# Kernel tuning notes

Measured on AMD Instinct MI355X. Metric: run time of the kernel, lower is better.

## Reference

```python
import jax, jax.numpy as jnp
import numpy as np

NX = 320   # image matrix (nRead)
NC = 8     # coils
NT = 8     # motion states
M = 65536  # non-Cartesian k-space samples per frame
OS = 2     # gridding oversampling factor


def setup_inputs() -> dict:
    key = jax.random.key(0)
    ks = jax.random.split(key, 7)
    kspace_r = jax.random.normal(ks[0], (NC, M), jnp.float32)
    kspace_i = jax.random.normal(ks[1], (NC, M), jnp.float32)
    # k-space trajectory normalized to [-0.5, 0.5)
    traj = jax.random.uniform(ks[2], (M, 2, NT), jnp.float32, -0.5, 0.5)
    csm_r = jax.random.normal(ks[3], (NC, NX, NX), jnp.float32)
    csm_i = jax.random.normal(ks[4], (NC, NX, NX), jnp.float32)
    dcf = jax.random.uniform(ks[5], (M, NT), jnp.float32)
    # motion/flow field in pixels, [NX, NX, 2, NT]
    motions = 3.0 * jax.random.normal(ks[6], (NX, NX, 2, NT), jnp.float32)
    return dict(kspace_r=kspace_r, kspace_i=kspace_i, traj=traj,
                csm_r=csm_r, csm_i=csm_i, dcf=dcf, motions=motions)


def _grid_adjoint(kspace, traj_t, dcf_t, csm):
    """Adjoint NUFFT (gpuNUFFT adj_op): density-compensated bilinear gridding
    onto a 2x oversampled Cartesian grid, inverse FFT, center crop,
    deapodization, and conjugate coil combination."""
    G = OS * NX
    data = (kspace * dcf_t[None, :]).astype(jnp.complex64)  # [NC, M]
    u = (traj_t[:, 0] + 0.5) * G
    v = (traj_t[:, 1] + 0.5) * G
    u0 = jnp.floor(u)
    v0 = jnp.floor(v)
    du = (u - u0).astype(jnp.float32)
    dv = (v - v0).astype(jnp.float32)
    i0 = u0.astype(jnp.int32) % G
    i1 = (i0 + 1) % G
    j0 = v0.astype(jnp.int32) % G
    j1 = (j0 + 1) % G
    grid = jnp.zeros((NC, G, G), jnp.complex64)
    grid = grid.at[:, i0, j0].add(data * ((1.0 - du) * (1.0 - dv)))
    grid = grid.at[:, i1, j0].add(data * (du * (1.0 - dv)))
    grid = grid.at[:, i0, j1].add(data * ((1.0 - du) * dv))
    grid = grid.at[:, i1, j1].add(data * (du * dv))
    im_os = jnp.fft.fftshift(
        jnp.fft.ifft2(jnp.fft.ifftshift(grid, axes=(-2, -1)), axes=(-2, -1)),
        axes=(-2, -1))
    s = (G - NX) // 2
    im = im_os[:, s:s + NX, s:s + NX]  # [NC, NX, NX]
    # deapodization: FT of the triangle (bilinear) gridding kernel is sinc^2
    x = (jnp.arange(NX, dtype=jnp.float32) - NX // 2) / G
    d = jnp.sinc(x) ** 2
    im = im / (d[:, None] * d[None, :])
    # conjugate coil combine with sensitivity maps
    return jnp.sum(jnp.conj(csm) * im, axis=0).astype(jnp.complex64)


def _bilinear_warp(im, flow):
    """apply_sparse_motion: sparse bilinear-interpolation warp of a 2D image
    by a per-pixel displacement field flow[..., 0:2] (in pixels)."""
    Nx, Ny = im.shape
    xs = jnp.arange(Nx, dtype=jnp.float32)[:, None] + flow[..., 0]
    ys = jnp.arange(Ny, dtype=jnp.float32)[None, :] + flow[..., 1]
    xs = jnp.clip(xs, 0.0, Nx - 1.0)
    ys = jnp.clip(ys, 0.0, Ny - 1.0)
    x0 = jnp.floor(xs).astype(jnp.int32)
    y0 = jnp.floor(ys).astype(jnp.int32)
    x1 = jnp.minimum(x0 + 1, Nx - 1)
    y1 = jnp.minimum(y0 + 1, Ny - 1)
    dx = xs - x0.astype(jnp.float32)
    dy = ys - y0.astype(jnp.float32)
    return ((1.0 - dx) * (1.0 - dy) * im[x0, y0]
            + dx * (1.0 - dy) * im[x1, y0]
            + (1.0 - dx) * dy * im[x0, y1]
            + dx * dy * im[x1, y1])


def reference(kspace_r, kspace_i, traj, csm_r, csm_i, dcf, motions):
    kspace = (kspace_r + 1j * kspace_i).astype(jnp.complex64)
    csm = (csm_r + 1j * csm_i).astype(jnp.complex64)

    def frame(traj_t, dcf_t, flow_t):
        im = _grid_adjoint(kspace, traj_t, dcf_t, csm)
        return _bilinear_warp(im, flow_t)

    # vmap over motion states: traj[..., t], dcf[..., t], motions[..., t]
    per_frame = jax.vmap(frame, in_axes=(2, 1, 3))(traj, dcf, motions)  # [NT, NX, NX]
    out = jnp.sum(per_frame, axis=0)  # temporal sum, complex [NX, NX]
    return jnp.stack([out.real, out.imag], axis=-1)  # [NX, NX, 2]
```

## Files before the change

### kernel.cpp

```cpp
#include <hip/hip_runtime.h>
#include <math.h>

#define NXI 320
#define NCI 8
#define NTI 8
#define MI  65536
#define GI  640
#define G2I (GI*GI)
#define NPIX (NXI*NXI)
#define REC_F 20
#define NBINS (NTI*G2I)
#define SCAN_BLKS (NBINS/1024)

typedef float v2f __attribute__((ext_vector_type(2)));

__device__ inline v2f cmul(v2f a, v2f b) {
    v2f axx = __builtin_shufflevector(a, a, 0, 0);
    v2f ayy = __builtin_shufflevector(a, a, 1, 1);
    v2f byx = __builtin_shufflevector(b, b, 1, 0);
    v2f r = axx * b;
    v2f t = ayy * byx;
    return r + v2f{-t.x, t.y};
}

__device__ inline v2f shfl_xor_v(v2f v, int m) {
    return v2f{__shfl_xor(v.x, m, 64), __shfl_xor(v.y, m, 64)};
}

__device__ inline void cell_of(const float* __restrict__ traj, int m, int f,
                               int& i0s, int& j0s, float& du, float& dv)
{
    float tu = traj[(m*2 + 0)*NTI + f];
    float tv = traj[(m*2 + 1)*NTI + f];
    float u = (tu + 0.5f) * (float)GI;
    float v = (tv + 0.5f) * (float)GI;
    float fu = floorf(u), fv = floorf(v);
    du = u - fu; dv = v - fv;
    i0s = (int)fu + GI/2; if (i0s >= GI) i0s -= GI;
    j0s = (int)fv + GI/2; if (j0s >= GI) j0s -= GI;
}

__global__ __launch_bounds__(256) void count_cells(
    const float* __restrict__ traj, int* __restrict__ counts)
{
    int tid = blockIdx.x * 256 + threadIdx.x;
    int f = tid >> 16, m = tid & (MI - 1);
    int i0s, j0s; float du, dv;
    cell_of(traj, m, f, i0s, j0s, du, dv);
    atomicAdd(&counts[f*G2I + i0s*GI + j0s], 1);
}

__device__ inline int scan1024(int v, int tid, int* tmp) {
    tmp[tid] = v; __syncthreads();
    for (int d = 1; d < 1024; d <<= 1) {
        int y = (tid >= d) ? tmp[tid - d] : 0;
        __syncthreads();
        tmp[tid] += y;
        __syncthreads();
    }
    return tmp[tid];
}

__global__ __launch_bounds__(1024) void scanA(const int* __restrict__ counts,
                                              int* __restrict__ binstart,
                                              int* __restrict__ sums)
{
    __shared__ int tmp[1024];
    int tid = threadIdx.x;
    int i = blockIdx.x * 1024 + tid;
    int v = counts[i];
    int incl = scan1024(v, tid, tmp);
    binstart[i] = incl - v;
    if (tid == 1023) sums[blockIdx.x] = incl;
}

__global__ __launch_bounds__(1024) void scanB(int* __restrict__ sums)
{
    __shared__ int tmp[1024];
    int tid = threadIdx.x;
    int base = tid * 4;
    int v[4]; int s = 0;
    #pragma unroll
    for (int q = 0; q < 4; ++q) {
        int idx = base + q;
        v[q] = (idx < SCAN_BLKS) ? sums[idx] : 0;
        s += v[q];
    }
    int incl = scan1024(s, tid, tmp);
    int run = incl - s;
    #pragma unroll
    for (int q = 0; q < 4; ++q) {
        int idx = base + q;
        if (idx < SCAN_BLKS) sums[idx] = run;
        run += v[q];
    }
}

__global__ __launch_bounds__(1024) void scanC(int* __restrict__ binstart,
                                              const int* __restrict__ sums,
                                              int* __restrict__ cursor)
{
    int i = blockIdx.x * 1024 + threadIdx.x;
    int v = binstart[i] + sums[blockIdx.x];
    binstart[i] = v;
    cursor[i] = v;
    if (i == NBINS - 1) binstart[NBINS] = NTI * MI;
}

__global__ __launch_bounds__(256) void scatter_cells(
    const float* __restrict__ kr, const float* __restrict__ ki,
    const float* __restrict__ traj, const float* __restrict__ dcf,
    int* __restrict__ cursor, float* __restrict__ recs)
{
    int tid = blockIdx.x * 256 + threadIdx.x;
    int f = tid >> 16, m = tid & (MI - 1);
    int i0s, j0s; float du, dv;
    cell_of(traj, m, f, i0s, j0s, du, dv);
    float w = dcf[m*NTI + f];
    int slot = atomicAdd(&cursor[f*G2I + i0s*GI + j0s], 1);
    float4* r = (float4*)(recs + (size_t)slot * REC_F);
    r[0] = make_float4(du, dv, 0.f, 0.f);
    #pragma unroll
    for (int q = 0; q < 4; ++q) {
        int c0 = 2*q;
        r[1+q] = make_float4(kr[c0*MI + m]*w,     ki[c0*MI + m]*w,
                             kr[(c0+1)*MI + m]*w, ki[(c0+1)*MI + m]*w);
    }
}

__device__ inline void dft5p(v2f x0, v2f x1, v2f x2, v2f x3, v2f x4, v2f* X)
{
    const float c1 = 0.309016994f, c2 = -0.809016994f;
    const float s1 = 0.951056516f, s2 =  0.587785252f;
    v2f S1 = x1 + x4, D1 = x1 - x4;
    v2f S2 = x2 + x3, D2 = x2 - x3;
    X[0] = x0 + S1 + S2;
    v2f A = x0 + c1*S1 + c2*S2;
    v2f T = s1*D1 + s2*D2;
    v2f B = x0 + c2*S1 + c1*S2;
    v2f U = s2*D1 - s1*D2;
    v2f iT = v2f{-T.y, T.x};
    v2f iU = v2f{-U.y, U.x};
    X[1] = A + iT;  X[4] = A - iT;
    X[2] = B + iU;  X[3] = B - iU;
}

__device__ inline void fft640_pruned(v2f* a, int lane, v2f* line, int xorm)
{
    const float PI = 3.14159265358979f;
    #pragma unroll
    for (int s = 0; s < 6; ++s) {
        const int h = 32 >> s;
        bool low = (lane & h) == 0;
        int k = (lane << s) & 63;
        float sn, cs;
        __sincosf((2.0f * PI / 64.0f) * (float)k, &sn, &cs);
        v2f ws = v2f{cs, sn};
        #pragma unroll
        for (int n = 0; n < 10; ++n) {
            v2f p = shfl_xor_v(a[n], h);
            v2f tl = p + a[n];
            v2f th = cmul(a[n] - p, ws);
            a[n] = low ? tl : th;
        }
    }
    int k1 = __brev(lane) >> 26;
    float th2 = (2.0f * PI / 640.0f) * (float)k1;
    float sn, cs;
    __sincosf(th2, &sn, &cs);
    v2f wb = v2f{cs, sn};
    v2f w = wb;
    #pragma unroll
    for (int n = 1; n < 10; ++n) {
        a[n] = cmul(a[n], w);
        w = cmul(w, wb);
    }
    v2f E[5], O[5];
    dft5p(a[0], a[2], a[4], a[6], a[8], E);
    dft5p(a[1], a[3], a[5], a[7], a[9], O);
    const v2f tk1 = { 0.809016994f, 0.587785252f};
    const v2f tk2 = { 0.309016994f, 0.951056516f};
    const v2f tk3 = {-0.309016994f, 0.951056516f};
    const v2f tk4 = {-0.809016994f, 0.587785252f};
    v2f t1 = cmul(tk1, O[1]);
    v2f t2 = cmul(tk2, O[2]);
    v2f t3 = cmul(tk3, O[3]);
    v2f t4 = cmul(tk4, O[4]);
    bool hi = (k1 >= 32);
    line[(160 + k1) ^ xorm] = E[0] + O[0];
    line[(224 + k1) ^ xorm] = E[1] + t1;
    int yx = hi ? (k1 - 32) : (288 + k1);
    v2f zx = hi ? (E[2] - t2) : (E[2] + t2);
    line[yx ^ xorm] = zx;
    line[(32 + k1) ^ xorm] = E[3] - t3;
    line[(96 + k1) ^ xorm] = E[4] - t4;
}

__global__ __launch_bounds__(512, 8) void row_fft(
    const int* __restrict__ binstart, const float* __restrict__ recs,
    v2f* __restrict__ rowout)
{
    __shared__ v2f A[NCI][GI];
    int bid = blockIdx.x;
    int i = bid % GI;
    int f = bid / GI;
    int tid = threadIdx.x;
    int im1 = i ? i - 1 : GI - 1;
    const int* bsr[2] = { binstart + f*G2I + i*GI,
                          binstart + f*G2I + im1*GI };

    for (int j = tid; j < GI; j += 512) {
        v2f acc[NCI];
        #pragma unroll
        for (int c = 0; c < NCI; ++c) acc[c] = v2f{0.f, 0.f};
        #pragma unroll
        for (int p = 0; p < 2; ++p) {
            const int* bs = bsr[p];
            if (j > 0) {
                int lo = bs[j-1], mid = bs[j], hi = bs[j+1];
                for (int s = lo; s < hi; ++s) {
                    const float4* R = (const float4*)(recs + (size_t)s*REC_F);
                    float4 h4 = R[0];
                    float wr = p ? h4.x : (1.f - h4.x);
                    float w  = wr * ((s < mid) ? h4.y : (1.f - h4.y));
                    float4 d0 = R[1], d1 = R[2], d2 = R[3], d3 = R[4];
                    acc[0] += w * v2f{d0.x, d0.y};  acc[1] += w * v2f{d0.z, d0.w};
                    acc[2] += w * v2f{d1.x, d1.y};  acc[3] += w * v2f{d1.z, d1.w};
                    acc[4] += w * v2f{d2.x, d2.y};  acc[5] += w * v2f{d2.z, d2.w};
                    acc[6] += w * v2f{d3.x, d3.y};  acc[7] += w * v2f{d3.z, d3.w};
                }
            } else {
                #pragma unroll
                for (int side = 0; side < 2; ++side) {
                    int b = side ? 0 : (GI - 1);
                    int s0 = bs[b], s1 = bs[b+1];
                    for (int s = s0; s < s1; ++s) {
                        const float4* R = (const float4*)(recs + (size_t)s*REC_F);
                        float4 h4 = R[0];
                        float wr = p ? h4.x : (1.f - h4.x);
                        float w  = wr * (side ? (1.f - h4.y) : h4.y);
                        float4 d0 = R[1], d1 = R[2], d2 = R[3], d3 = R[4];
                        acc[0] += w * v2f{d0.x, d0.y};  acc[1] += w * v2f{d0.z, d0.w};
                        acc[2] += w * v2f{d1.x, d1.y};  acc[3] += w * v2f{d1.z, d1.w};
                        acc[4] += w * v2f{d2.x, d2.y};  acc[5] += w * v2f{d2.z, d2.w};
                        acc[6] += w * v2f{d3.x, d3.y};  acc[7] += w * v2f{d3.z, d3.w};
                    }
                }
            }
        }
        #pragma unroll
        for (int c = 0; c < NCI; ++c) A[c][j] = acc[c];
    }
    __syncthreads();

    int wv = tid >> 6, lane = tid & 63;
    v2f a[10];
    #pragma unroll
    for (int n = 0; n < 10; ++n) a[n] = A[wv][10*lane + n];
    fft640_pruned(a, lane, A[wv], 0);
    v2f* dst = rowout + (((size_t)f*NCI + wv)*GI + i)*NXI;
    #pragma unroll
    for (int q = 0; q < 5; ++q) {
        int yc = lane + 64*q;
        dst[yc] = A[wv][yc];
    }
}

__global__ __launch_bounds__(512, 8) void col_fft(
    const v2f* __restrict__ rowout, v2f* __restrict__ colimg)
{
    __shared__ v2f A[8][GI];
    int bid = blockIdx.x;
    int g = bid % 40;
    int c = (bid / 40) % NCI;
    int f = bid / (40*NCI);
    int y0 = g * 8;
    int tid = threadIdx.x;
    const v2f* src = rowout + ((size_t)f*NCI + c)*GI*NXI + y0;
    for (int idx = tid; idx < 8*GI; idx += 512) {
        int l = idx & 7, k = idx >> 3;
        A[l][k ^ (4*(l & 3))] = src[(size_t)k*NXI + l];
    }
    __syncthreads();
    int wv = tid >> 6, lane = tid & 63;
    int xm = 4 * (wv & 3);
    v2f a[10];
    #pragma unroll
    for (int n = 0; n < 10; ++n) a[n] = A[wv][(10*lane + n) ^ xm];
    fft640_pruned(a, lane, A[wv], xm);
    __syncthreads();
    v2f* dst = colimg + ((size_t)f*NCI + c)*NPIX + y0;
    for (int idx = tid; idx < 8*NXI; idx += 512) {
        int l = idx & 7, xx = idx >> 3;
        dst[(size_t)xx*NXI + l] = A[l][xx ^ (4*(l & 3))];
    }
}

__global__ __launch_bounds__(256) void combine_kernel(
    const float2* __restrict__ colimg, const float* __restrict__ csr,
    const float* __restrict__ csi, float2* __restrict__ img)
{
    int f = blockIdx.y;
    int pix = blockIdx.x * 256 + threadIdx.x;
    int x = pix / NXI, y = pix - x*NXI;
    const float PI = 3.14159265358979f;
    float tx = (x - 160) * (1.0f/GI);
    float ty = (y - 160) * (1.0f/GI);
    float dx = 1.0f, dy = 1.0f;
    if (x != 160) { float s = __sinf(PI*tx) / (PI*tx); dx = s*s; }
    if (y != 160) { float s = __sinf(PI*ty) / (PI*ty); dy = s*s; }
    float scale = 1.0f / ((float)G2I * dx * dy);
    float accr = 0.f, acci = 0.f;
    #pragma unroll
    for (int c = 0; c < NCI; ++c) {
        float2 g = colimg[((size_t)f*NCI + c)*NPIX + pix];
        float cr = csr[c*NPIX + pix];
        float ci = csi[c*NPIX + pix];
        accr += cr*g.x + ci*g.y;
        acci += cr*g.y - ci*g.x;
    }
    img[(size_t)f*NPIX + pix] = make_float2(accr*scale, acci*scale);
}

__global__ __launch_bounds__(256) void warp_sum(
    const float2* __restrict__ img, const float* __restrict__ motions,
    float* __restrict__ out)
{
    int pix = blockIdx.x * 256 + threadIdx.x;
    int x = pix / NXI, y = pix - x*NXI;
    float accr = 0.f, acci = 0.f;
    #pragma unroll
    for (int f = 0; f < NTI; ++f) {
        float fx = motions[(size_t)(pix*2 + 0)*NTI + f];
        float fy = motions[(size_t)(pix*2 + 1)*NTI + f];
        float xs = fminf(fmaxf((float)x + fx, 0.0f), (float)(NXI-1));
        float ys = fminf(fmaxf((float)y + fy, 0.0f), (float)(NXI-1));
        int x0 = (int)floorf(xs);
        int y0 = (int)floorf(ys);
        int x1 = min(x0+1, NXI-1);
        int y1 = min(y0+1, NXI-1);
        float dx = xs - (float)x0;
        float dy = ys - (float)y0;
        const float2* im = img + (size_t)f*NPIX;
        float2 v00 = im[x0*NXI + y0];
        float2 v10 = im[x1*NXI + y0];
        float2 v01 = im[x0*NXI + y1];
        float2 v11 = im[x1*NXI + y1];
        float w00 = (1.f-dx)*(1.f-dy), w10 = dx*(1.f-dy);
        float w01 = (1.f-dx)*dy,       w11 = dx*dy;
        accr += w00*v00.x + w10*v10.x + w01*v01.x + w11*v11.x;
        acci += w00*v00.y + w10*v10.y + w01*v01.y + w11*v11.y;
    }
    out[pix*2+0] = accr;
    out[pix*2+1] = acci;
}

extern "C" void kernel_launch(void* const* d_in, const int* in_sizes, int n_in,
                              void* d_out, int out_size, void* d_ws, size_t ws_size,
                              hipStream_t stream)
{
    const float* kr   = (const float*)d_in[0];
    const float* ki   = (const float*)d_in[1];
    const float* traj = (const float*)d_in[2];
    const float* csr  = (const float*)d_in[3];
    const float* csi  = (const float*)d_in[4];
    const float* dcf  = (const float*)d_in[5];
    const float* mot  = (const float*)d_in[6];
    float* out = (float*)d_out;

    char* ws = (char*)d_ws;
    float*  recs     = (float*)ws;
    ws += (size_t)NTI * MI * REC_F * sizeof(float);
    v2f*    rowout   = (v2f*)ws;
    ws += (size_t)NTI * NCI * GI * NXI * sizeof(float2);
    float2* colimg   = (float2*)ws;
    ws += (size_t)NTI * NCI * NPIX * sizeof(float2);
    float2* img      = (float2*)ws;
    ws += (size_t)NTI * NPIX * sizeof(float2);
    int*    counts   = (int*)ws;  ws += (size_t)NBINS * sizeof(int);
    int*    binstart = (int*)ws;  ws += ((size_t)NBINS + 16) * sizeof(int);
    int*    cursor   = (int*)ws;  ws += (size_t)NBINS * sizeof(int);
    int*    sums     = (int*)ws;  ws += (size_t)SCAN_BLKS * sizeof(int);

    hipMemsetAsync(counts, 0, (size_t)NBINS * sizeof(int), stream);
    count_cells  <<<NTI*MI/256, 256, 0, stream>>>(traj, counts);
    scanA        <<<SCAN_BLKS, 1024, 0, stream>>>(counts, binstart, sums);
    scanB        <<<1,         1024, 0, stream>>>(sums);
    scanC        <<<SCAN_BLKS, 1024, 0, stream>>>(binstart, sums, cursor);
    scatter_cells<<<NTI*MI/256, 256, 0, stream>>>(kr, ki, traj, dcf, cursor, recs);
    row_fft      <<<NTI*GI,     512, 0, stream>>>(binstart, recs, rowout);
    col_fft      <<<NTI*NCI*40, 512, 0, stream>>>(rowout, (v2f*)colimg);
    combine_kernel<<<dim3(NPIX/256, NTI), 256, 0, stream>>>(colimg, csr, csi, img);
    warp_sum     <<<NPIX/256,   256, 0, stream>>>(img, mot, out);
}
```

Baseline: 306.9 us.

## Fuse binning pipeline into one cooperative kernel with grid syncs

Replaces the memset, count, three scan kernels and the scatter kernel with a single cooperative kernel that uses grid-wide syncs between phases. The count phase reads the trajectory and dcf per sample with vectorized loads and writes transposed copies, which the scatter phase then reads with coalesced access. This removes several kernel launches and the strided trajectory reads, but adds grid.sync costs and confines the whole binning stage to 256 blocks of 1024 threads. In the count phase only 64 of those blocks have any work.

```diff
diff --git a/kernel.cpp b/kernel.cpp
--- a/kernel.cpp
+++ b/kernel.cpp
@@ -1,5 +1,8 @@
 #include <hip/hip_runtime.h>
+#include <hip/hip_cooperative_groups.h>
 #include <math.h>
+
+namespace cg = cooperative_groups;
 
 #define NXI 320
 #define NCI 8
@@ -11,6 +14,9 @@
 #define REC_F 20
 #define NBINS (NTI*G2I)
 #define SCAN_BLKS (NBINS/1024)
+#define COOP_BLKS 256
+#define COOP_THR  1024
+#define COOP_TOT  (COOP_BLKS*COOP_THR)
 
 typedef float v2f __attribute__((ext_vector_type(2)));
 
@@ -27,29 +33,6 @@
     return v2f{__shfl_xor(v.x, m, 64), __shfl_xor(v.y, m, 64)};
 }
 
-__device__ inline void cell_of(const float* __restrict__ traj, int m, int f,
-                               int& i0s, int& j0s, float& du, float& dv)
-{
-    float tu = traj[(m*2 + 0)*NTI + f];
-    float tv = traj[(m*2 + 1)*NTI + f];
-    float u = (tu + 0.5f) * (float)GI;
-    float v = (tv + 0.5f) * (float)GI;
-    float fu = floorf(u), fv = floorf(v);
-    du = u - fu; dv = v - fv;
-    i0s = (int)fu + GI/2; if (i0s >= GI) i0s -= GI;
-    j0s = (int)fv + GI/2; if (j0s >= GI) j0s -= GI;
-}
-
-__global__ __launch_bounds__(256) void count_cells(
-    const float* __restrict__ traj, int* __restrict__ counts)
-{
-    int tid = blockIdx.x * 256 + threadIdx.x;
-    int f = tid >> 16, m = tid & (MI - 1);
-    int i0s, j0s; float du, dv;
-    cell_of(traj, m, f, i0s, j0s, du, dv);
-    atomicAdd(&counts[f*G2I + i0s*GI + j0s], 1);
-}
-
 __device__ inline int scan1024(int v, int tid, int* tmp) {
     tmp[tid] = v; __syncthreads();
     for (int d = 1; d < 1024; d <<= 1) {
@@ -61,70 +44,105 @@
     return tmp[tid];
 }
 
-__global__ __launch_bounds__(1024) void scanA(const int* __restrict__ counts,
-                                              int* __restrict__ binstart,
-                                              int* __restrict__ sums)
-{
-    __shared__ int tmp[1024];
-    int tid = threadIdx.x;
-    int i = blockIdx.x * 1024 + tid;
-    int v = counts[i];
-    int incl = scan1024(v, tid, tmp);
-    binstart[i] = incl - v;
-    if (tid == 1023) sums[blockIdx.x] = incl;
-}
-
-__global__ __launch_bounds__(1024) void scanB(int* __restrict__ sums)
-{
-    __shared__ int tmp[1024];
-    int tid = threadIdx.x;
-    int base = tid * 4;
-    int v[4]; int s = 0;
-    #pragma unroll
-    for (int q = 0; q < 4; ++q) {
-        int idx = base + q;
-        v[q] = (idx < SCAN_BLKS) ? sums[idx] : 0;
-        s += v[q];
-    }
-    int incl = scan1024(s, tid, tmp);
-    int run = incl - s;
-    #pragma unroll
-    for (int q = 0; q < 4; ++q) {
-        int idx = base + q;
-        if (idx < SCAN_BLKS) sums[idx] = run;
-        run += v[q];
-    }
-}
-
-__global__ __launch_bounds__(1024) void scanC(int* __restrict__ binstart,
-                                              const int* __restrict__ sums,
-                                              int* __restrict__ cursor)
-{
-    int i = blockIdx.x * 1024 + threadIdx.x;
-    int v = binstart[i] + sums[blockIdx.x];
-    binstart[i] = v;
-    cursor[i] = v;
-    if (i == NBINS - 1) binstart[NBINS] = NTI * MI;
-}
-
-__global__ __launch_bounds__(256) void scatter_cells(
+__global__ __launch_bounds__(COOP_THR, 4) void bin_coop(
+    const float4* __restrict__ traj4, const float4* __restrict__ dcf4,
     const float* __restrict__ kr, const float* __restrict__ ki,
-    const float* __restrict__ traj, const float* __restrict__ dcf,
-    int* __restrict__ cursor, float* __restrict__ recs)
-{
-    int tid = blockIdx.x * 256 + threadIdx.x;
-    int f = tid >> 16, m = tid & (MI - 1);
-    int i0s, j0s; float du, dv;
-    cell_of(traj, m, f, i0s, j0s, du, dv);
-    float w = dcf[m*NTI + f];
-    int slot = atomicAdd(&cursor[f*G2I + i0s*GI + j0s], 1);
-    float4* r = (float4*)(recs + (size_t)slot * REC_F);
-    r[0] = make_float4(du, dv, 0.f, 0.f);
-    #pragma unroll
-    for (int q = 0; q < 4; ++q) {
-        int c0 = 2*q;
-        r[1+q] = make_float4(kr[c0*MI + m]*w,     ki[c0*MI + m]*w,
-                             kr[(c0+1)*MI + m]*w, ki[(c0+1)*MI + m]*w);
+    int* __restrict__ counts, int* __restrict__ binstart,
+    int* __restrict__ cursor, int* __restrict__ sums,
+    float* __restrict__ trajT, float* __restrict__ dcfT,
+    float* __restrict__ recs)
+{
+    cg::grid_group grid = cg::this_grid();
+    __shared__ int tmp[COOP_THR];
+    const int tid = threadIdx.x;
+    const int gid = blockIdx.x * COOP_THR + tid;
+
+    {
+        int4* c4 = (int4*)counts;
+        for (int i = gid; i < NBINS/4; i += COOP_TOT) c4[i] = make_int4(0,0,0,0);
+    }
+    grid.sync();
+
+    if (gid < MI) {
+        int m = gid;
+        float4 t0 = traj4[m*4+0], t1 = traj4[m*4+1];
+        float4 t2 = traj4[m*4+2], t3 = traj4[m*4+3];
+        float4 d0 = dcf4[m*2+0],  d1 = dcf4[m*2+1];
+        float u[8]  = {t0.x,t0.y,t0.z,t0.w, t1.x,t1.y,t1.z,t1.w};
+        float v[8]  = {t2.x,t2.y,t2.z,t2.w, t3.x,t3.y,t3.z,t3.w};
+        float dd[8] = {d0.x,d0.y,d0.z,d0.w, d1.x,d1.y,d1.z,d1.w};
+        #pragma unroll
+        for (int f = 0; f < NTI; ++f) {
+            trajT[(f*2+0)*MI + m] = u[f];
+            trajT[(f*2+1)*MI + m] = v[f];
+            dcfT[f*MI + m] = dd[f];
+            float uu = (u[f] + 0.5f) * (float)GI;
+            float vv = (v[f] + 0.5f) * (float)GI;
+            int i0 = (int)floorf(uu) + GI/2; if (i0 >= GI) i0 -= GI;
+            int j0 = (int)floorf(vv) + GI/2; if (j0 >= GI) j0 -= GI;
+            atomicAdd(&counts[f*G2I + i0*GI + j0], 1);
+        }
+    }
+    grid.sync();
+
+    for (int vb = blockIdx.x; vb < SCAN_BLKS; vb += COOP_BLKS) {
+        __syncthreads();
+        int i = vb*1024 + tid;
+        int v = counts[i];
+        int incl = scan1024(v, tid, tmp);
+        binstart[i] = incl - v;
+        if (tid == 1023) sums[vb] = incl;
+    }
+    grid.sync();
+
+    if (blockIdx.x == 0) {
+        int base = tid * 4;
+        int v[4]; int s = 0;
+        #pragma unroll
+        for (int q = 0; q < 4; ++q) {
+            int idx = base + q;
+            v[q] = (idx < SCAN_BLKS) ? sums[idx] : 0;
+            s += v[q];
+        }
+        int incl = scan1024(s, tid, tmp);
+        int run = incl - s;
+        #pragma unroll
+        for (int q = 0; q < 4; ++q) {
+            int idx = base + q;
+            if (idx < SCAN_BLKS) sums[idx] = run;
+            run += v[q];
+        }
+    }
+    grid.sync();
+
+    for (int i = gid; i < NBINS; i += COOP_TOT) {
+        int v = binstart[i] + sums[i >> 10];
+        binstart[i] = v;
+        cursor[i] = v;
+    }
+    if (gid == 0) binstart[NBINS] = NTI * MI;
+    grid.sync();
+
+    for (int g2 = gid; g2 < NTI*MI; g2 += COOP_TOT) {
+        int f = g2 >> 16, m = g2 & (MI - 1);
+        float tu = trajT[(f*2+0)*MI + m];
+        float tv = trajT[(f*2+1)*MI + m];
+        float w  = dcfT[f*MI + m];
+        float uu = (tu + 0.5f) * (float)GI;
+        float vv = (tv + 0.5f) * (float)GI;
+        float fu = floorf(uu), fv = floorf(vv);
+        float du = uu - fu, dv = vv - fv;
+        int i0s = (int)fu + GI/2; if (i0s >= GI) i0s -= GI;
+        int j0s = (int)fv + GI/2; if (j0s >= GI) j0s -= GI;
+        int slot = atomicAdd(&cursor[f*G2I + i0s*GI + j0s], 1);
+        float4* r = (float4*)(recs + (size_t)slot * REC_F);
+        r[0] = make_float4(du, dv, 0.f, 0.f);
+        #pragma unroll
+        for (int q = 0; q < 4; ++q) {
+            int c0 = 2*q;
+            r[1+q] = make_float4(kr[c0*MI + m]*w,     ki[c0*MI + m]*w,
+                                 kr[(c0+1)*MI + m]*w, ki[(c0+1)*MI + m]*w);
+        }
     }
 }
 
@@ -380,14 +398,21 @@
     int*    counts   = (int*)ws;  ws += (size_t)NBINS * sizeof(int);
     int*    binstart = (int*)ws;  ws += ((size_t)NBINS + 16) * sizeof(int);
     int*    cursor   = (int*)ws;  ws += (size_t)NBINS * sizeof(int);
-    int*    sums     = (int*)ws;  ws += (size_t)SCAN_BLKS * sizeof(int);
-
-    hipMemsetAsync(counts, 0, (size_t)NBINS * sizeof(int), stream);
-    count_cells  <<<NTI*MI/256, 256, 0, stream>>>(traj, counts);
-    scanA        <<<SCAN_BLKS, 1024, 0, stream>>>(counts, binstart, sums);
-    scanB        <<<1,         1024, 0, stream>>>(sums);
-    scanC        <<<SCAN_BLKS, 1024, 0, stream>>>(binstart, sums, cursor);
-    scatter_cells<<<NTI*MI/256, 256, 0, stream>>>(kr, ki, traj, dcf, cursor, recs);
+    int*    sums     = (int*)ws;  ws += 16384;
+    float*  trajT    = (float*)ws; ws += (size_t)NTI * 2 * MI * sizeof(float);
+    float*  dcfT     = (float*)ws; ws += (size_t)NTI * MI * sizeof(float);
+
+    const float4* traj4 = (const float4*)traj;
+    const float4* dcf4  = (const float4*)dcf;
+
+    void* kargs[] = {
+        (void*)&traj4, (void*)&dcf4, (void*)&kr, (void*)&ki,
+        (void*)&counts, (void*)&binstart, (void*)&cursor, (void*)&sums,
+        (void*)&trajT, (void*)&dcfT, (void*)&recs
+    };
+    hipLaunchCooperativeKernel((void*)bin_coop, dim3(COOP_BLKS), dim3(COOP_THR),
+                               kargs, 0, stream);
+
     row_fft      <<<NTI*GI,     512, 0, stream>>>(binstart, recs, rowout);
     col_fft      <<<NTI*NCI*40, 512, 0, stream>>>(rowout, (v2f*)colimg);
     combine_kernel<<<dim3(NPIX/256, NTI), 256, 0, stream>>>(colimg, csr, csi, img);
```

New measurement: 482.4 us. 1.57x slower.

## Drop scanC pass by adding block offsets on the fly and reuse counts as cursor

Applied to the files above, without the earlier changes.

Removes the scanC kernel that wrote global bin offsets and a cursor array. Block-level sums are now added where offsets are read, in scatter_cells and row_fft, and scatter slots come from atomically decrementing counts. This saves a full pass over about 3.3M bins, one launch and a cursor buffer, at the cost of an extra sums lookup per bin read. The radix-2 FFT butterfly is also rewritten branch-free with a sign vector and unit twiddle.

```diff
diff --git a/kernel.cpp b/kernel.cpp
--- a/kernel.cpp
+++ b/kernel.cpp
@@ -74,7 +74,8 @@
     if (tid == 1023) sums[blockIdx.x] = incl;
 }
 
-__global__ __launch_bounds__(1024) void scanB(int* __restrict__ sums)
+__global__ __launch_bounds__(1024) void scanB(int* __restrict__ sums,
+                                              int* __restrict__ binstart)
 {
     __shared__ int tmp[1024];
     int tid = threadIdx.x;
@@ -94,30 +95,26 @@
         if (idx < SCAN_BLKS) sums[idx] = run;
         run += v[q];
     }
-}
-
-__global__ __launch_bounds__(1024) void scanC(int* __restrict__ binstart,
-                                              const int* __restrict__ sums,
-                                              int* __restrict__ cursor)
-{
-    int i = blockIdx.x * 1024 + threadIdx.x;
-    int v = binstart[i] + sums[blockIdx.x];
-    binstart[i] = v;
-    cursor[i] = v;
-    if (i == NBINS - 1) binstart[NBINS] = NTI * MI;
+    if (tid == SCAN_BLKS/4 - 1) {
+        sums[SCAN_BLKS] = run;
+        binstart[NBINS] = 0;
+    }
 }
 
 __global__ __launch_bounds__(256) void scatter_cells(
     const float* __restrict__ kr, const float* __restrict__ ki,
     const float* __restrict__ traj, const float* __restrict__ dcf,
-    int* __restrict__ cursor, float* __restrict__ recs)
+    int* __restrict__ counts, const int* __restrict__ binstart,
+    const int* __restrict__ sums, float* __restrict__ recs)
 {
     int tid = blockIdx.x * 256 + threadIdx.x;
     int f = tid >> 16, m = tid & (MI - 1);
     int i0s, j0s; float du, dv;
     cell_of(traj, m, f, i0s, j0s, du, dv);
     float w = dcf[m*NTI + f];
-    int slot = atomicAdd(&cursor[f*G2I + i0s*GI + j0s], 1);
+    int bin = f*G2I + i0s*GI + j0s;
+    int within = atomicSub(&counts[bin], 1) - 1;
+    int slot = binstart[bin] + sums[bin >> 10] + within;
     float4* r = (float4*)(recs + (size_t)slot * REC_F);
     r[0] = make_float4(du, dv, 0.f, 0.f);
     #pragma unroll
@@ -152,16 +149,17 @@
     for (int s = 0; s < 6; ++s) {
         const int h = 32 >> s;
         bool low = (lane & h) == 0;
-        int k = (lane << s) & 63;
+        int kp = (lane << s) & 31;
         float sn, cs;
-        __sincosf((2.0f * PI / 64.0f) * (float)k, &sn, &cs);
-        v2f ws = v2f{cs, sn};
+        __sincosf((2.0f * PI / 64.0f) * (float)kp, &sn, &cs);
+        v2f w = low ? v2f{1.f, 0.f} : v2f{cs, sn};
+        float sg = low ? 1.f : -1.f;
+        v2f sgv = v2f{sg, sg};
         #pragma unroll
         for (int n = 0; n < 10; ++n) {
             v2f p = shfl_xor_v(a[n], h);
-            v2f tl = p + a[n];
-            v2f th = cmul(a[n] - p, ws);
-            a[n] = low ? tl : th;
+            v2f t = sgv * a[n] + p;
+            a[n] = cmul(t, w);
         }
     }
     int k1 = __brev(lane) >> 26;
@@ -197,8 +195,8 @@
 }
 
 __global__ __launch_bounds__(512, 8) void row_fft(
-    const int* __restrict__ binstart, const float* __restrict__ recs,
-    v2f* __restrict__ rowout)
+    const int* __restrict__ binstart, const int* __restrict__ sums,
+    const float* __restrict__ recs, v2f* __restrict__ rowout)
 {
     __shared__ v2f A[NCI][GI];
     int bid = blockIdx.x;
@@ -206,8 +204,10 @@
     int f = bid / GI;
     int tid = threadIdx.x;
     int im1 = i ? i - 1 : GI - 1;
-    const int* bsr[2] = { binstart + f*G2I + i*GI,
-                          binstart + f*G2I + im1*GI };
+    const int base0 = f*G2I + i*GI;
+    const int base1 = f*G2I + im1*GI;
+
+    #define GS(b) (binstart[b] + sums[(b) >> 10])
 
     for (int j = tid; j < GI; j += 512) {
         v2f acc[NCI];
@@ -215,9 +215,9 @@
         for (int c = 0; c < NCI; ++c) acc[c] = v2f{0.f, 0.f};
         #pragma unroll
         for (int p = 0; p < 2; ++p) {
-            const int* bs = bsr[p];
+            const int base = p ? base1 : base0;
             if (j > 0) {
-                int lo = bs[j-1], mid = bs[j], hi = bs[j+1];
+                int lo = GS(base + j - 1), mid = GS(base + j), hi = GS(base + j + 1);
                 for (int s = lo; s < hi; ++s) {
                     const float4* R = (const float4*)(recs + (size_t)s*REC_F);
                     float4 h4 = R[0];
@@ -232,8 +232,8 @@
             } else {
                 #pragma unroll
                 for (int side = 0; side < 2; ++side) {
-                    int b = side ? 0 : (GI - 1);
-                    int s0 = bs[b], s1 = bs[b+1];
+                    int b = base + (side ? 0 : (GI - 1));
+                    int s0 = GS(b), s1 = GS(b + 1);
                     for (int s = s0; s < s1; ++s) {
                         const float4* R = (const float4*)(recs + (size_t)s*REC_F);
                         float4 h4 = R[0];
@@ -251,6 +251,7 @@
         #pragma unroll
         for (int c = 0; c < NCI; ++c) A[c][j] = acc[c];
     }
+    #undef GS
     __syncthreads();
 
     int wv = tid >> 6, lane = tid & 63;
@@ -379,16 +380,15 @@
     ws += (size_t)NTI * NPIX * sizeof(float2);
     int*    counts   = (int*)ws;  ws += (size_t)NBINS * sizeof(int);
     int*    binstart = (int*)ws;  ws += ((size_t)NBINS + 16) * sizeof(int);
-    int*    cursor   = (int*)ws;  ws += (size_t)NBINS * sizeof(int);
-    int*    sums     = (int*)ws;  ws += (size_t)SCAN_BLKS * sizeof(int);
+    int*    sums     = (int*)ws;  ws += 16384;
 
     hipMemsetAsync(counts, 0, (size_t)NBINS * sizeof(int), stream);
     count_cells  <<<NTI*MI/256, 256, 0, stream>>>(traj, counts);
     scanA        <<<SCAN_BLKS, 1024, 0, stream>>>(counts, binstart, sums);
-    scanB        <<<1,         1024, 0, stream>>>(sums);
-    scanC        <<<SCAN_BLKS, 1024, 0, stream>>>(binstart, sums, cursor);
-    scatter_cells<<<NTI*MI/256, 256, 0, stream>>>(kr, ki, traj, dcf, cursor, recs);
-    row_fft      <<<NTI*GI,     512, 0, stream>>>(binstart, recs, rowout);
+    scanB        <<<1,         1024, 0, stream>>>(sums, binstart);
+    scatter_cells<<<NTI*MI/256, 256, 0, stream>>>(kr, ki, traj, dcf, counts,
+                                                  binstart, sums, recs);
+    row_fft      <<<NTI*GI,     512, 0, stream>>>(binstart, sums, recs, rowout);
     col_fft      <<<NTI*NCI*40, 512, 0, stream>>>(rowout, (v2f*)colimg);
     combine_kernel<<<dim3(NPIX/256, NTI), 256, 0, stream>>>(colimg, csr, csi, img);
     warp_sum     <<<NPIX/256,   256, 0, stream>>>(img, mot, out);
```

New measurement: 304.5 us. No clear change (-0.8%).
